# Optimization experiments

Measured on AMD Instinct MI355X. Metric: run time of the kernel, lower is better.

## Reference

```python
import jax, jax.numpy as jnp
import numpy as np
from jax import lax

RATIOS = (0.5, 1.0, 2.0)
SCALES = (8, 16, 32)
BASE = 16
STRIDE = 16
NMS_THRESH = 0.7
N_PRE = 6000   # n_test_pre_nms
N_POST = 300   # n_test_post_nms
MIN_SIZE = 16.0  # min_size * scale (scale=1.0)
NEG = -1e9


def _anchor_base():
    py = px = BASE / 2.0
    ab = np.zeros((len(RATIOS) * len(SCALES), 4), np.float32)
    for i, r in enumerate(RATIOS):
        for j, s in enumerate(SCALES):
            h = BASE * s * np.sqrt(r)
            w = BASE * s * np.sqrt(1.0 / r)
            k = i * len(SCALES) + j
            ab[k] = [py - h / 2.0, px - w / 2.0, py + h / 2.0, px + w / 2.0]
    return ab


def _anchors(hh, ww):
    # enumerate shifted anchors, shape [hh*ww*9, 4] in (y1,x1,y2,x2)
    ab = _anchor_base()
    sy = np.arange(hh, dtype=np.float32) * STRIDE
    sx = np.arange(ww, dtype=np.float32) * STRIDE
    sx, sy = np.meshgrid(sx, sy)
    shift = np.stack([sy.ravel(), sx.ravel(), sy.ravel(), sx.ravel()], axis=1)
    a = (ab[None, :, :] + shift[:, None, :]).reshape(-1, 4).astype(np.float32)
    return jnp.asarray(a)


def _conv(x, w, b, pad):
    y = lax.conv_general_dilated(x, w, (1, 1), [(pad, pad), (pad, pad)],
                                 dimension_numbers=('NCHW', 'OIHW', 'NCHW'))
    return y + b[None, :, None, None]


def _nms(boxes, valid):
    # greedy NMS over score-sorted boxes [N,4]; returns N_POST selected indices (-1 = pad)
    N = boxes.shape[0]
    y1, x1, y2, x2 = boxes[:, 0], boxes[:, 1], boxes[:, 2], boxes[:, 3]
    area = (y2 - y1) * (x2 - x1)
    idx = jnp.arange(N)

    def body(i, sup):
        cur = valid[i] & (~sup[i])
        ih = jnp.clip(jnp.minimum(y2[i], y2) - jnp.maximum(y1[i], y1), 0.0)
        iw = jnp.clip(jnp.minimum(x2[i], x2) - jnp.maximum(x1[i], x1), 0.0)
        inter = ih * iw
        iou = inter / (area[i] + area - inter + 1e-9)
        return sup | (cur & (iou > NMS_THRESH) & (idx > i))

    sup = lax.fori_loop(0, N, body, jnp.zeros((N,), bool))
    kept = valid & (~sup)
    rank = jnp.cumsum(kept) - 1
    sel = jnp.full((N_POST,), -1, jnp.int32)
    sel = sel.at[jnp.where(kept & (rank < N_POST), rank, N_POST)].set(
        jnp.arange(N, dtype=jnp.int32), mode='drop')
    return sel


def setup_inputs() -> dict:
    key = jax.random.key(0)
    ks = jax.random.split(key, 5)
    n, c, hh, ww = 8, 512, 64, 64
    x = jax.random.normal(ks[0], (n, c, hh, ww), jnp.float32)
    # normal_init(mean=0, std=0.01), biases zero
    w1 = 0.01 * jax.random.normal(ks[1], (512, 512, 3, 3), jnp.float32)
    b1 = jnp.zeros((512,), jnp.float32)
    w_score = 0.01 * jax.random.normal(ks[2], (18, 512, 1, 1), jnp.float32)
    b_score = jnp.zeros((18,), jnp.float32)
    w_loc = 0.01 * jax.random.normal(ks[3], (36, 512, 1, 1), jnp.float32)
    b_loc = jnp.zeros((36,), jnp.float32)
    return {"x": x, "w1": w1, "b1": b1, "w_score": w_score, "b_score": b_score,
            "w_loc": w_loc, "b_loc": b_loc, "img_h": 1024, "img_w": 1024}


def reference(x, w1, b1, w_score, b_score, w_loc, b_loc, img_h, img_w):
    n, _, hh, ww = x.shape
    anchor = _anchors(hh, ww)  # [K,4]
    mid = jax.nn.relu(_conv(x, w1, b1, 1))
    rpn_locs = _conv(mid, w_loc, b_loc, 0).transpose(0, 2, 3, 1).reshape(n, -1, 4)  # [n,K,4]
    raw = _conv(mid, w_score, b_score, 0).transpose(0, 2, 3, 1)  # [n,hh,ww,18]
    sm = jax.nn.softmax(raw.reshape(n, hh, ww, -1, 2), axis=-1)
    fg = sm[..., 1].reshape(n, -1)          # [n,K] foreground scores
    rpn_scores = raw.reshape(n, -1, 2)      # pre-softmax, as in original
    # loc2bbox decode
    ah = anchor[:, 2] - anchor[:, 0]
    aw = anchor[:, 3] - anchor[:, 1]
    acy = anchor[:, 0] + 0.5 * ah
    acx = anchor[:, 1] + 0.5 * aw
    dy, dx, dh, dw = (rpn_locs[..., 0], rpn_locs[..., 1], rpn_locs[..., 2], rpn_locs[..., 3])
    cy = dy * ah + acy
    cx = dx * aw + acx
    h = ah * jnp.exp(dh)
    w = aw * jnp.exp(dw)
    fh = jnp.float32(img_h)
    fw = jnp.float32(img_w)
    roi = jnp.stack([jnp.clip(cy - 0.5 * h, 0.0, fh), jnp.clip(cx - 0.5 * w, 0.0, fw),
                     jnp.clip(cy + 0.5 * h, 0.0, fh), jnp.clip(cx + 0.5 * w, 0.0, fw)], axis=-1)
    hs = roi[..., 2] - roi[..., 0]
    ws = roi[..., 3] - roi[..., 1]
    ok = (hs >= MIN_SIZE) & (ws >= MIN_SIZE)
    masked = jnp.where(ok, fg, NEG)
    vals, top = lax.top_k(masked, N_PRE)  # score-descending pre-NMS selection
    boxes = jnp.take_along_axis(roi, top[..., None], axis=1)  # [n,N_PRE,4]
    valid = vals > NEG / 2
    sel = jax.vmap(_nms)(boxes, valid)  # [n,N_POST]
    mask = sel >= 0
    rois = jnp.take_along_axis(boxes, jnp.clip(sel, 0)[..., None], axis=1)
    rois = jnp.where(mask[..., None], rois, 0.0)  # [n,N_POST,4], zero-padded
    roi_indices = jnp.where(mask, jnp.arange(n, dtype=jnp.int32)[:, None], -1)  # -1 = pad
    return (rpn_locs, rpn_scores, rois, roi_indices, anchor)
```

## Files before the change

### kernel.cpp

```cpp
#include <hip/hip_runtime.h>
#include <cstdint>
#include <cstddef>

#define CIN 512
#define NA 36864
#define NPRE 6000
#define NPOST 300
#define CBUF_CAP 8192
#define NWORD 94
#define NEGV -1000000000.0f
#define ISTRIDE 76

#define O_LOCS   0
#define O_SCORES 1179648
#define O_ROIS   1769472
#define O_RIDX   1779072
#define O_ANCH   1781472

__device__ __forceinline__ float fmulr(float a, float b) { return __fmul_rn(a, b); }
__device__ __forceinline__ float faddr(float a, float b) { return __fadd_rn(a, b); }
__device__ __forceinline__ float fsubr(float a, float b) { return __fsub_rn(a, b); }

__device__ __forceinline__ void anchor_for(int a, int pos, float* anc) {
    const double rat[3] = {0.5, 1.0, 2.0};
    const double scl[3] = {8.0, 16.0, 32.0};
    int ri = a / 3, si = a - ri * 3;
    double h = 16.0 * scl[si] * sqrt(rat[ri]);
    double w = 16.0 * scl[si] * sqrt(1.0 / rat[ri]);
    float a0 = (float)(8.0 - h * 0.5);
    float a1 = (float)(8.0 - w * 0.5);
    float a2 = (float)(8.0 + h * 0.5);
    float a3 = (float)(8.0 + w * 0.5);
    int y = pos >> 6, x = pos & 63;
    float sy = (float)(y * 16), sx = (float)(x * 16);
    anc[0] = faddr(a0, sy); anc[1] = faddr(a1, sx);
    anc[2] = faddr(a2, sy); anc[3] = faddr(a3, sx);
}

__device__ __forceinline__ bool decode_box(float4 L, const float* anc, float* box) {
    float ah  = fsubr(anc[2], anc[0]);
    float aw  = fsubr(anc[3], anc[1]);
    float acy = faddr(anc[0], fmulr(0.5f, ah));
    float acx = faddr(anc[1], fmulr(0.5f, aw));
    float cy  = faddr(fmulr(L.x, ah), acy);
    float cx  = faddr(fmulr(L.y, aw), acx);
    float h   = fmulr(ah, expf(L.z));
    float w   = fmulr(aw, expf(L.w));
    float y1 = fminf(fmaxf(fsubr(cy, fmulr(0.5f, h)), 0.0f), 1024.0f);
    float x1 = fminf(fmaxf(fsubr(cx, fmulr(0.5f, w)), 0.0f), 1024.0f);
    float y2 = fminf(fmaxf(faddr(cy, fmulr(0.5f, h)), 0.0f), 1024.0f);
    float x2 = fminf(fmaxf(faddr(cx, fmulr(0.5f, w)), 0.0f), 1024.0f);
    box[0] = y1; box[1] = x1; box[2] = y2; box[3] = x2;
    float hs = fsubr(y2, y1), ws2 = fsubr(x2, x1);
    return (hs >= 16.0f) && (ws2 >= 16.0f);
}

__device__ __forceinline__ unsigned long long mono64(double f) {
    unsigned long long u = (unsigned long long)__double_as_longlong(f);
    return (u & 0x8000000000000000ull) ? ~u : (u | 0x8000000000000000ull);
}

__global__ __launch_bounds__(256) void k_wreord(const float* __restrict__ w1,
                                                float* __restrict__ wr2) {
    __shared__ float tile[64][37];
    const int ct0 = blockIdx.x * 36;
    const int ocb = blockIdx.y;
    const int t = threadIdx.x;
    for (int i = t; i < 64 * 36; i += 256) {
        int orow = i / 36, c = i - orow * 36;
        tile[orow][c] = w1[(size_t)(ocb * 64 + orow) * 4608 + ct0 + c];
    }
    __syncthreads();
    for (int i = t; i < 36 * 64; i += 256) {
        int ct = i >> 6, o = i & 63;
        wr2[((size_t)ocb * 4608 + ct0 + ct) * 64 + o] = tile[o][ct];
    }
}

__global__ __launch_bounds__(256, 2) void k_conv3(const float* __restrict__ x,
                                                  const float* __restrict__ wr2,
                                                  const float* __restrict__ b1,
                                                  float* __restrict__ mid) {
    __shared__ float in_s[8 * 6 * ISTRIDE];
    __shared__ float w_s[8 * 9 * 64];
    const int yb  = blockIdx.x;
    const int ocb = blockIdx.y;
    const int n   = blockIdx.z;
    const int t   = threadIdx.x;
    const int y0  = yb * 4;
    const int tocg = t >> 5;
    const int tx   = t & 31;
    const int r    = tx >> 3;
    const int xo   = (tx & 7) << 3;

    for (int i = t; i < 48 * 8; i += 256) {
        int row = i >> 3, c = i & 7;
        int xi = (c < 4) ? c : 64 + c;
        in_s[row * ISTRIDE + xi] = 0.f;
    }

    int   ilds[3];
    int   ival[3];
    const float* igp[3];
#pragma unroll
    for (int k = 0; k < 3; ++k) {
        int s = t + k * 256;
        int row = s >> 4, col = s & 15;
        int cc = row / 6, rr = row - cc * 6;
        int gy = y0 - 1 + rr;
        ival[k] = (gy >= 0 && gy < 64) ? 1 : 0;
        int gyc = min(max(gy, 0), 63);
        ilds[k] = row * ISTRIDE + 4 + col * 4;
        igp[k]  = x + (((size_t)(n * CIN + cc) * 64 + gyc) * 64 + col * 4);
    }
    const float* wgp = wr2 + (size_t)ocb * (4608 * 64);

    float acc[8][8];
#pragma unroll
    for (int i = 0; i < 8; i++)
#pragma unroll
        for (int j = 0; j < 8; j++) acc[i][j] = 0.f;

    for (int ch = 0; ch < 64; ++ch) {
        const float* wp0 = wgp + (size_t)ch * 4608;
#pragma unroll
        for (int k = 0; k < 4; ++k)
            *(float4*)&w_s[4 * t + 1024 * k] = *(const float4*)(wp0 + 4 * t + 1024 * k);
        if (t < 128)
            *(float4*)&w_s[4 * t + 4096] = *(const float4*)(wp0 + 4 * t + 4096);
#pragma unroll
        for (int k = 0; k < 3; ++k) {
            float4 v = make_float4(0.f, 0.f, 0.f, 0.f);
            if (ival[k]) v = *(const float4*)(igp[k] + (size_t)ch * 32768);
            *(float4*)&in_s[ilds[k]] = v;
        }
        __syncthreads();

        float sub[8][8];
#pragma unroll
        for (int i = 0; i < 8; i++)
#pragma unroll
            for (int j = 0; j < 8; j++) sub[i][j] = 0.f;
#pragma unroll 1
        for (int cc = 0; cc < 8; ++cc) {
#pragma unroll
            for (int dy = 0; dy < 3; ++dy) {
                const float4* ip =
                    (const float4*)&in_s[cc * (6 * ISTRIDE) + (r + dy) * ISTRIDE + xo];
                float4 Q0 = ip[0], Q1 = ip[1], Q2 = ip[2], Q3 = ip[3];
                float in16[16] = {Q0.x, Q0.y, Q0.z, Q0.w, Q1.x, Q1.y, Q1.z, Q1.w,
                                  Q2.x, Q2.y, Q2.z, Q2.w, Q3.x, Q3.y, Q3.z, Q3.w};
#pragma unroll
                for (int dx = 0; dx < 3; ++dx) {
                    const float4* wp =
                        (const float4*)&w_s[cc * 576 + (dy * 3 + dx) * 64 + tocg * 8];
                    float4 W0 = wp[0], W1 = wp[1];
                    float w8[8] = {W0.x, W0.y, W0.z, W0.w, W1.x, W1.y, W1.z, W1.w};
#pragma unroll
                    for (int i = 0; i < 8; i++)
#pragma unroll
                        for (int j = 0; j < 8; j++)
                            sub[i][j] += w8[i] * in16[j + dx + 3];
                }
            }
        }
#pragma unroll
        for (int i = 0; i < 8; i++)
#pragma unroll
            for (int j = 0; j < 8; j++) acc[i][j] += sub[i][j];
        __syncthreads();
    }
    const int ocbase = (ocb << 6) + tocg * 8;
#pragma unroll
    for (int i = 0; i < 8; i++) {
        float bb = b1[ocbase + i];
#pragma unroll
        for (int j = 0; j < 8; j++) {
            float v = fmaxf(acc[i][j] + bb, 0.f);
            mid[((n * CIN + ocbase + i) * 64 + (y0 + r)) * 64 + xo + j] = v;
        }
    }
}

__global__ __launch_bounds__(256) void k_conv1(const float* __restrict__ mid,
                                               const float* __restrict__ wl,
                                               const float* __restrict__ bl,
                                               const float* __restrict__ wsc,
                                               const float* __restrict__ bs,
                                               float* __restrict__ out,
                                               double* __restrict__ fgbuf) {
    __shared__ float in_s[128 * 64];
    __shared__ float w_s[54 * 128];
    const int y = blockIdx.x;
    const int n = blockIdx.y;
    const int t = threadIdx.x;
    const int xx = t & 63, og = t >> 6;
    double accd[14];
#pragma unroll
    for (int k = 0; k < 14; k++) accd[k] = 0.0;

    for (int c0 = 0; c0 < 512; c0 += 128) {
        for (int idx = t; idx < 128 * 64; idx += 256) {
            int cc = idx >> 6, x2 = idx & 63;
            in_s[idx] = mid[((n * CIN + c0 + cc) * 64 + y) * 64 + x2];
        }
        for (int idx = t; idx < 54 * 128; idx += 256) {
            int oc = idx >> 7, cc = idx & 127;
            w_s[idx] = (oc < 36) ? wl[oc * 512 + c0 + cc] : wsc[(oc - 36) * 512 + c0 + cc];
        }
        __syncthreads();
#pragma unroll 1
        for (int cc = 0; cc < 128; ++cc) {
            double iv = (double)in_s[cc * 64 + xx];
#pragma unroll
            for (int k = 0; k < 14; k++) {
                int oc = og * 14 + k;
                if (oc < 54) accd[k] += (double)w_s[oc * 128 + cc] * iv;
            }
        }
        __syncthreads();
    }
    const int pos = y * 64 + xx;
    double sv[14];
#pragma unroll
    for (int k = 0; k < 14; k++) {
        int oc = og * 14 + k;
        if (oc >= 54) break;
        if (oc < 36) {
            double v = accd[k] + (double)bl[oc];
            int a = oc >> 2, cd = oc & 3;
            out[O_LOCS + ((size_t)(n * NA + pos * 9 + a)) * 4 + cd] = (float)v;
        } else {
            sv[k] = accd[k] + (double)bs[oc - 36];
            int c2 = oc - 36, a = c2 >> 1, cls = c2 & 1;
            out[O_SCORES + ((size_t)(n * NA + pos * 9 + a)) * 2 + cls] = (float)sv[k];
        }
    }
#pragma unroll
    for (int k = 0; k < 13; k++) {
        int oc = og * 14 + k;
        if (oc >= 36 && oc < 54 && ((oc - 36) & 1) == 0) {
            double s0 = sv[k], s1 = sv[k + 1];
            double m = fmax(s0, s1);
            double e0 = exp(s0 - m), e1 = exp(s1 - m);
            double fg = e1 / (e0 + e1);
            int a = (oc - 36) >> 1;
            fgbuf[(size_t)n * NA + pos * 9 + a] = fg;
        }
    }
}

__global__ __launch_bounds__(256) void k_keys(const float* __restrict__ out,
                                              const double* __restrict__ fgbuf,
                                              unsigned long long* __restrict__ keys) {
    const int n = blockIdx.x / 144;
    const int i = (blockIdx.x % 144) * 256 + threadIdx.x;
    int pos = i / 9, a = i - pos * 9;
    float anc[4]; anchor_for(a, pos, anc);
    float4 L = *(const float4*)&out[O_LOCS + (size_t)(n * NA + i) * 4];
    float box[4];
    bool ok = decode_box(L, anc, box);
    double f = ok ? fgbuf[(size_t)n * NA + i] : (double)NEGV;
    unsigned long long m = mono64(f);
    keys[(size_t)n * NA + i] =
        (m & 0xFFFFFFFFFFFF0000ull) | (unsigned long long)(0xFFFFu - (unsigned)i);
}

__global__ __launch_bounds__(1024) void k_select(const unsigned long long* __restrict__ keys,
                                                 unsigned long long* __restrict__ kth) {
    __shared__ unsigned int hist[8192];
    __shared__ unsigned int gs[256];
    __shared__ unsigned long long s_pref;
    __shared__ int s_plen, s_rem;
    const int n = blockIdx.x, t = threadIdx.x;
    if (t == 0) { s_pref = 0ull; s_plen = 0; s_rem = NPRE; }
    __syncthreads();
    const int shifts[5] = {51, 38, 25, 12, 0};
    const int widths[5] = {13, 13, 13, 13, 12};
    for (int lev = 0; lev < 5; ++lev) {
        const int nb = 1 << widths[lev];
        for (int b = t; b < nb; b += 1024) hist[b] = 0;
        __syncthreads();
        const unsigned long long pref = s_pref;
        const int plen = s_plen;
        for (int i = t; i < NA; i += 1024) {
            unsigned long long key = keys[(size_t)n * NA + i];
            if (plen == 0 || (key >> (64 - plen)) == pref) {
                unsigned int bin = (unsigned int)((key >> shifts[lev]) & (unsigned)(nb - 1));
                atomicAdd(&hist[bin], 1u);
            }
        }
        __syncthreads();
        const int gsz = nb >> 8;
        if (t < 256) {
            unsigned int s = 0;
            for (int m = 0; m < gsz; m++) s += hist[t * gsz + m];
            gs[t] = s;
        }
        __syncthreads();
        if (t == 0) {
            const unsigned int rem = (unsigned int)s_rem;
            unsigned int acc = 0; int selbin = 0;
            for (int g = 255; g >= 0; --g) {
                if (acc + gs[g] >= rem) {
                    for (int b = g * gsz + gsz - 1; b >= g * gsz; --b) {
                        if (acc + hist[b] >= rem) { selbin = b; break; }
                        acc += hist[b];
                    }
                    break;
                }
                acc += gs[g];
            }
            s_rem = (int)(rem - acc);
            s_pref = (s_pref << widths[lev]) | (unsigned long long)(unsigned)selbin;
            s_plen += widths[lev];
        }
        __syncthreads();
    }
    if (t == 0) kth[n] = s_pref;
}

__global__ void k_compact(const unsigned long long* __restrict__ keys,
                          const unsigned long long* __restrict__ kth,
                          unsigned long long* __restrict__ cbuf,
                          unsigned int* __restrict__ cnt) {
    const int n = blockIdx.x / 144;
    const int i = (blockIdx.x % 144) * 256 + threadIdx.x;
    unsigned long long key = keys[(size_t)n * NA + i];
    if (key >= kth[n]) {
        unsigned int p = atomicAdd(&cnt[n], 1u);
        if (p < CBUF_CAP) cbuf[(size_t)n * CBUF_CAP + p] = key;
    }
}

__global__ __launch_bounds__(1024) void k_sort(const unsigned long long* __restrict__ cbuf,
                                               const float* __restrict__ out,
                                               float* __restrict__ bsort,
                                               unsigned char* __restrict__ vflag) {
    __shared__ unsigned long long arr[CBUF_CAP];
    const int n = blockIdx.x, t = threadIdx.x;
    for (int idx = t; idx < CBUF_CAP; idx += 1024)
        arr[idx] = (idx < NPRE) ? cbuf[(size_t)n * CBUF_CAP + idx] : 0ull;
    __syncthreads();
    for (int k = 2; k <= CBUF_CAP; k <<= 1)
        for (int j = k >> 1; j > 0; j >>= 1) {
            for (int i = t; i < CBUF_CAP; i += 1024) {
                int ixj = i ^ j;
                if (ixj > i) {
                    unsigned long long a = arr[i], b = arr[ixj];
                    bool up = (i & k) == 0;
                    if (up ? (a < b) : (a > b)) { arr[i] = b; arr[ixj] = a; }
                }
            }
            __syncthreads();
        }
    for (int r = t; r < NPRE; r += 1024) {
        unsigned long long key = arr[r];
        unsigned int i = 0xFFFFu - (unsigned int)(key & 0xFFFFull);
        int pos = i / 9, a = i - pos * 9;
        float anc[4]; anchor_for(a, pos, anc);
        float4 L = *(const float4*)&out[O_LOCS + (size_t)(n * NA + i) * 4];
        float box[4];
        bool ok = decode_box(L, anc, box);
        ((float4*)bsort)[(size_t)n * NPRE + r] = make_float4(box[0], box[1], box[2], box[3]);
        vflag[(size_t)n * NPRE + r] = ok ? 1 : 0;
    }
}

__global__ __launch_bounds__(256) void k_mask(const float* __restrict__ bsort,
                                              unsigned long long* __restrict__ masks) {
    __shared__ float4 bx[1024];
    const int n  = blockIdx.z;
    const int jc = blockIdx.y;
    const int i  = blockIdx.x * 256 + threadIdx.x;
    const bool have = i < NPRE;
    float4 bi = make_float4(0, 0, 0, 0); float areai = 0.f;
    if (have) {
        bi = ((const float4*)bsort)[(size_t)n * NPRE + i];
        areai = fmulr(fsubr(bi.z, bi.x), fsubr(bi.w, bi.y));
    }
    const int jn = min(1024, NPRE - jc * 1024);
    for (int jj = threadIdx.x; jj < jn; jj += 256)
        bx[jj] = ((const float4*)bsort)[(size_t)n * NPRE + jc * 1024 + jj];
    __syncthreads();
    for (int w = 0; w < 16; ++w) {
        int gw = jc * 16 + w;
        if (gw >= NWORD) break;
        unsigned long long m = 0ull;
        int jbase = jc * 1024 + w * 64;
        if (have && jbase + 63 > i) {
#pragma unroll 1
            for (int b = 0; b < 64; b++) {
                int j = jbase + b;
                if (j > i && j < NPRE) {
                    float4 bj = bx[w * 64 + b];
                    float ih = fmaxf(fsubr(fminf(bi.z, bj.z), fmaxf(bi.x, bj.x)), 0.f);
                    float iw = fmaxf(fsubr(fminf(bi.w, bj.w), fmaxf(bi.y, bj.y)), 0.f);
                    float inter = fmulr(ih, iw);
                    float areaj = fmulr(fsubr(bj.z, bj.x), fsubr(bj.w, bj.y));
                    float den = faddr(fsubr(faddr(areai, areaj), inter), 1e-9f);
                    float iou = __fdiv_rn(inter, den);
                    if (iou > 0.7f) m |= (1ull << b);
                }
            }
        }
        if (have) masks[((size_t)n * NPRE + i) * NWORD + gw] = m;
    }
}

__global__ __launch_bounds__(128) void k_scan(const unsigned long long* __restrict__ masks,
                                              const unsigned char* __restrict__ vflag,
                                              const float* __restrict__ bsort,
                                              float* __restrict__ out) {
    __shared__ unsigned long long sup[NWORD];
    __shared__ unsigned long long valw[NWORD];
    __shared__ int kept;
    const int n = blockIdx.x, t = threadIdx.x;
    if (t == 0) kept = 0;
    if (t < NWORD) {
        sup[t] = 0ull;
        unsigned long long v = 0ull;
        for (int b = 0; b < 64; b++) {
            int r = t * 64 + b;
            if (r < NPRE && vflag[(size_t)n * NPRE + r]) v |= (1ull << b);
        }
        valw[t] = v;
    }
    __syncthreads();
    for (int i = 0; i < NPRE; ++i) {
        bool keep = ((valw[i >> 6] >> (i & 63)) & 1ull) && !((sup[i >> 6] >> (i & 63)) & 1ull);
        if (keep) {
            if (t < NWORD) sup[t] |= masks[((size_t)n * NPRE + i) * NWORD + t];
            if (t == 0) {
                int r = kept;
                if (r < NPOST) {
                    float4 b4 = ((const float4*)bsort)[(size_t)n * NPRE + i];
                    out[O_ROIS + (size_t)(n * NPOST + r) * 4 + 0] = b4.x;
                    out[O_ROIS + (size_t)(n * NPOST + r) * 4 + 1] = b4.y;
                    out[O_ROIS + (size_t)(n * NPOST + r) * 4 + 2] = b4.z;
                    out[O_ROIS + (size_t)(n * NPOST + r) * 4 + 3] = b4.w;
                    out[O_RIDX + n * NPOST + r] = (float)n;
                }
                kept = r + 1;
            }
            __syncthreads();
            if (kept >= NPOST) break;
        }
    }
    __syncthreads();
    for (int r = kept + t; r < NPOST; r += 128) {
        out[O_ROIS + (size_t)(n * NPOST + r) * 4 + 0] = 0.f;
        out[O_ROIS + (size_t)(n * NPOST + r) * 4 + 1] = 0.f;
        out[O_ROIS + (size_t)(n * NPOST + r) * 4 + 2] = 0.f;
        out[O_ROIS + (size_t)(n * NPOST + r) * 4 + 3] = 0.f;
        out[O_RIDX + n * NPOST + r] = -1.0f;
    }
}

__global__ void k_anchor(float* __restrict__ out) {
    int i = blockIdx.x * 256 + threadIdx.x;
    if (i >= NA) return;
    int pos = i / 9, a = i - pos * 9;
    float anc[4]; anchor_for(a, pos, anc);
    out[O_ANCH + (size_t)i * 4 + 0] = anc[0];
    out[O_ANCH + (size_t)i * 4 + 1] = anc[1];
    out[O_ANCH + (size_t)i * 4 + 2] = anc[2];
    out[O_ANCH + (size_t)i * 4 + 3] = anc[3];
}

extern "C" void kernel_launch(void* const* d_in, const int* in_sizes, int n_in,
                              void* d_out, int out_size, void* d_ws, size_t ws_size,
                              hipStream_t stream) {
    const float* x   = (const float*)d_in[0];
    const float* w1  = (const float*)d_in[1];
    const float* b1  = (const float*)d_in[2];
    const float* wsc = (const float*)d_in[3];
    const float* bsc = (const float*)d_in[4];
    const float* wlc = (const float*)d_in[5];
    const float* blc = (const float*)d_in[6];
    float* out = (float*)d_out;
    char* ws = (char*)d_ws;

    float* wr2                = (float*)(ws + 0);
    float* mid                = (float*)(ws + 9437184);
    double* fgbuf             = (double*)(ws + 76546048);
    unsigned long long* keys  = (unsigned long long*)(ws + 78905344);
    unsigned long long* kth   = (unsigned long long*)(ws + 81264640);
    unsigned int* cnt         = (unsigned int*)(ws + 81265152);
    unsigned long long* cbuf  = (unsigned long long*)(ws + 81265664);
    float* bsort              = (float*)(ws + 81789952);
    unsigned char* vflag      = (unsigned char*)(ws + 82557952);
    unsigned long long* masks = (unsigned long long*)(ws + 82606080);

    hipMemsetAsync(cnt, 0, 8 * 4, stream);

    dim3 gw(128, 8);
    k_wreord<<<gw, 256, 0, stream>>>(w1, wr2);
    dim3 g3(16, 8, 8);
    k_conv3<<<g3, 256, 0, stream>>>(x, wr2, b1, mid);
    dim3 g1(64, 8);
    k_conv1<<<g1, 256, 0, stream>>>(mid, wlc, blc, wsc, bsc, out, fgbuf);
    k_keys<<<1152, 256, 0, stream>>>(out, fgbuf, keys);
    k_select<<<8, 1024, 0, stream>>>(keys, kth);
    k_compact<<<1152, 256, 0, stream>>>(keys, kth, cbuf, cnt);
    k_sort<<<8, 1024, 0, stream>>>(cbuf, out, bsort, vflag);
    dim3 gm(24, 6, 8);
    k_mask<<<gm, 256, 0, stream>>>(bsort, masks);
    k_scan<<<8, 128, 0, stream>>>(masks, vflag, bsort, out);
    k_anchor<<<144, 256, 0, stream>>>(out);
}
```

Measured before the change: 2.998 ms.

## Fuse top-k select/compact/sort kernels and rewrite NMS scan as single-wavefront ballot loop

Merges the radix select, compaction and bitonic sort into one k_topk kernel that reuses a shared-memory union, and folds anchor output into k_keys, which removes several launches and the memset. The radix bin search now uses a parallel suffix scan over group sums in place of a serial loop. The NMS scan kernel becomes one 64-lane wavefront that keeps valid and suppressed bitmasks in registers and uses ballot/ffs to jump straight to the next kept box, avoiding a walk over all 6000 candidates with block syncs. The remaining cost is the 8-block serial tail, and the compaction now uses a global atomic counter that is reset inside the kernel.

After: 3.002 ms. About the same (+0.1%).

```diff
diff --git a/kernel.cpp b/kernel.cpp
--- a/kernel.cpp
+++ b/kernel.cpp
@@ -6,7 +6,7 @@
 #define NA 36864
 #define NPRE 6000
 #define NPOST 300
-#define CBUF_CAP 8192
+#define NARR 8192
 #define NWORD 94
 #define NEGV -1000000000.0f
 #define ISTRIDE 76
@@ -250,39 +250,53 @@
     }
 }
 
-__global__ __launch_bounds__(256) void k_keys(const float* __restrict__ out,
+__global__ __launch_bounds__(256) void k_keys(const float* __restrict__ out_ro,
                                               const double* __restrict__ fgbuf,
-                                              unsigned long long* __restrict__ keys) {
+                                              unsigned long long* __restrict__ keys,
+                                              float* __restrict__ out) {
     const int n = blockIdx.x / 144;
     const int i = (blockIdx.x % 144) * 256 + threadIdx.x;
     int pos = i / 9, a = i - pos * 9;
     float anc[4]; anchor_for(a, pos, anc);
-    float4 L = *(const float4*)&out[O_LOCS + (size_t)(n * NA + i) * 4];
+    float4 L = *(const float4*)&out_ro[O_LOCS + (size_t)(n * NA + i) * 4];
     float box[4];
     bool ok = decode_box(L, anc, box);
     double f = ok ? fgbuf[(size_t)n * NA + i] : (double)NEGV;
     unsigned long long m = mono64(f);
     keys[(size_t)n * NA + i] =
         (m & 0xFFFFFFFFFFFF0000ull) | (unsigned long long)(0xFFFFu - (unsigned)i);
-}
-
-__global__ __launch_bounds__(1024) void k_select(const unsigned long long* __restrict__ keys,
-                                                 unsigned long long* __restrict__ kth) {
-    __shared__ unsigned int hist[8192];
-    __shared__ unsigned int gs[256];
-    __shared__ unsigned long long s_pref;
-    __shared__ int s_plen, s_rem;
+    if (blockIdx.x < 144) {
+        out[O_ANCH + (size_t)i * 4 + 0] = anc[0];
+        out[O_ANCH + (size_t)i * 4 + 1] = anc[1];
+        out[O_ANCH + (size_t)i * 4 + 2] = anc[2];
+        out[O_ANCH + (size_t)i * 4 + 3] = anc[3];
+    }
+}
+
+__global__ __launch_bounds__(1024) void k_topk(const unsigned long long* __restrict__ keys,
+                                               const float* __restrict__ out,
+                                               unsigned int* __restrict__ cntg,
+                                               float* __restrict__ bsort,
+                                               unsigned char* __restrict__ vflag) {
+    __shared__ union SM {
+        unsigned int hist[16384];
+        unsigned long long arr[NARR];
+    } sm;
     const int n = blockIdx.x, t = threadIdx.x;
-    if (t == 0) { s_pref = 0ull; s_plen = 0; s_rem = NPRE; }
+    unsigned int* hist = sm.hist;
+    unsigned int* gs = sm.hist + 8192;
+    unsigned long long* prefp = (unsigned long long*)&sm.hist[8452];
+    if (t == 0) { hist[8448] = NPRE; *prefp = 0ull; }
     __syncthreads();
     const int shifts[5] = {51, 38, 25, 12, 0};
     const int widths[5] = {13, 13, 13, 13, 12};
+    int plen = 0;
     for (int lev = 0; lev < 5; ++lev) {
         const int nb = 1 << widths[lev];
+        const int gsz = nb >> 8;
         for (int b = t; b < nb; b += 1024) hist[b] = 0;
         __syncthreads();
-        const unsigned long long pref = s_pref;
-        const int plen = s_plen;
+        const unsigned long long pref = *prefp;
         for (int i = t; i < NA; i += 1024) {
             unsigned long long key = keys[(size_t)n * NA + i];
             if (plen == 0 || (key >> (64 - plen)) == pref) {
@@ -291,60 +305,57 @@
             }
         }
         __syncthreads();
-        const int gsz = nb >> 8;
         if (t < 256) {
             unsigned int s = 0;
             for (int m = 0; m < gsz; m++) s += hist[t * gsz + m];
             gs[t] = s;
         }
         __syncthreads();
+        for (int off = 1; off < 256; off <<= 1) {
+            unsigned int v = 0;
+            if (t < 256 && t + off < 256) v = gs[t + off];
+            __syncthreads();
+            if (t < 256) gs[t] += v;
+            __syncthreads();
+        }
+        const unsigned int rem = hist[8448];
+        if (t < 256) {
+            unsigned int here = gs[t];
+            unsigned int above = (t == 255) ? 0u : gs[t + 1];
+            if (here >= rem && above < rem) hist[8449] = (unsigned int)t;
+        }
+        __syncthreads();
         if (t == 0) {
-            const unsigned int rem = (unsigned int)s_rem;
-            unsigned int acc = 0; int selbin = 0;
-            for (int g = 255; g >= 0; --g) {
-                if (acc + gs[g] >= rem) {
-                    for (int b = g * gsz + gsz - 1; b >= g * gsz; --b) {
-                        if (acc + hist[b] >= rem) { selbin = b; break; }
-                        acc += hist[b];
-                    }
-                    break;
-                }
-                acc += gs[g];
+            int G = (int)hist[8449];
+            unsigned int acc = (G == 255) ? 0u : gs[G + 1];
+            int selbin = G * gsz;
+            for (int b = G * gsz + gsz - 1; b >= G * gsz; --b) {
+                if (acc + hist[b] >= rem) { selbin = b; break; }
+                acc += hist[b];
             }
-            s_rem = (int)(rem - acc);
-            s_pref = (s_pref << widths[lev]) | (unsigned long long)(unsigned)selbin;
-            s_plen += widths[lev];
-        }
-        __syncthreads();
-    }
-    if (t == 0) kth[n] = s_pref;
-}
-
-__global__ void k_compact(const unsigned long long* __restrict__ keys,
-                          const unsigned long long* __restrict__ kth,
-                          unsigned long long* __restrict__ cbuf,
-                          unsigned int* __restrict__ cnt) {
-    const int n = blockIdx.x / 144;
-    const int i = (blockIdx.x % 144) * 256 + threadIdx.x;
-    unsigned long long key = keys[(size_t)n * NA + i];
-    if (key >= kth[n]) {
-        unsigned int p = atomicAdd(&cnt[n], 1u);
-        if (p < CBUF_CAP) cbuf[(size_t)n * CBUF_CAP + p] = key;
-    }
-}
-
-__global__ __launch_bounds__(1024) void k_sort(const unsigned long long* __restrict__ cbuf,
-                                               const float* __restrict__ out,
-                                               float* __restrict__ bsort,
-                                               unsigned char* __restrict__ vflag) {
-    __shared__ unsigned long long arr[CBUF_CAP];
-    const int n = blockIdx.x, t = threadIdx.x;
-    for (int idx = t; idx < CBUF_CAP; idx += 1024)
-        arr[idx] = (idx < NPRE) ? cbuf[(size_t)n * CBUF_CAP + idx] : 0ull;
+            hist[8448] = rem - acc;
+            *prefp = ((*prefp) << widths[lev]) | (unsigned long long)(unsigned)selbin;
+        }
+        plen += widths[lev];
+        __syncthreads();
+    }
+    const unsigned long long kth = *prefp;
+    if (t == 0) cntg[n] = 0u;
     __syncthreads();
-    for (int k = 2; k <= CBUF_CAP; k <<= 1)
+    unsigned long long* arr = sm.arr;
+    for (int i = t; i < NA; i += 1024) {
+        unsigned long long key = keys[(size_t)n * NA + i];
+        if (key >= kth) {
+            unsigned int p = atomicAdd(&cntg[n], 1u);
+            if (p < NARR) arr[p] = key;
+        }
+    }
+    __syncthreads();
+    for (int idx = NPRE + t; idx < NARR; idx += 1024) arr[idx] = 0ull;
+    __syncthreads();
+    for (int k = 2; k <= NARR; k <<= 1)
         for (int j = k >> 1; j > 0; j >>= 1) {
-            for (int i = t; i < CBUF_CAP; i += 1024) {
+            for (int i = t; i < NARR; i += 1024) {
                 int ixj = i ^ j;
                 if (ixj > i) {
                     unsigned long long a = arr[i], b = arr[ixj];
@@ -408,64 +419,60 @@
     }
 }
 
-__global__ __launch_bounds__(128) void k_scan(const unsigned long long* __restrict__ masks,
-                                              const unsigned char* __restrict__ vflag,
-                                              const float* __restrict__ bsort,
-                                              float* __restrict__ out) {
-    __shared__ unsigned long long sup[NWORD];
-    __shared__ unsigned long long valw[NWORD];
-    __shared__ int kept;
-    const int n = blockIdx.x, t = threadIdx.x;
-    if (t == 0) kept = 0;
-    if (t < NWORD) {
-        sup[t] = 0ull;
-        unsigned long long v = 0ull;
-        for (int b = 0; b < 64; b++) {
-            int r = t * 64 + b;
-            if (r < NPRE && vflag[(size_t)n * NPRE + r]) v |= (1ull << b);
-        }
-        valw[t] = v;
-    }
-    __syncthreads();
-    for (int i = 0; i < NPRE; ++i) {
-        bool keep = ((valw[i >> 6] >> (i & 63)) & 1ull) && !((sup[i >> 6] >> (i & 63)) & 1ull);
-        if (keep) {
-            if (t < NWORD) sup[t] |= masks[((size_t)n * NPRE + i) * NWORD + t];
-            if (t == 0) {
-                int r = kept;
-                if (r < NPOST) {
-                    float4 b4 = ((const float4*)bsort)[(size_t)n * NPRE + i];
-                    out[O_ROIS + (size_t)(n * NPOST + r) * 4 + 0] = b4.x;
-                    out[O_ROIS + (size_t)(n * NPOST + r) * 4 + 1] = b4.y;
-                    out[O_ROIS + (size_t)(n * NPOST + r) * 4 + 2] = b4.z;
-                    out[O_ROIS + (size_t)(n * NPOST + r) * 4 + 3] = b4.w;
-                    out[O_RIDX + n * NPOST + r] = (float)n;
-                }
-                kept = r + 1;
-            }
-            __syncthreads();
-            if (kept >= NPOST) break;
-        }
-    }
-    __syncthreads();
-    for (int r = kept + t; r < NPOST; r += 128) {
+__global__ __launch_bounds__(64) void k_scan(const unsigned long long* __restrict__ masks,
+                                             const unsigned char* __restrict__ vflag,
+                                             const float* __restrict__ bsort,
+                                             float* __restrict__ out) {
+    const int n = blockIdx.x;
+    const int l = threadIdx.x;
+    unsigned long long valw0 = 0ull, valw1 = 0ull;
+    for (int w = 0; w < NWORD; ++w) {
+        int idx = w * 64 + l;
+        bool v = (idx < NPRE) && (vflag[(size_t)n * NPRE + idx] != 0);
+        unsigned long long word = __ballot(v);
+        if (w == l) valw0 = word;
+        if (w == 64 + l) valw1 = word;
+    }
+    unsigned long long sup0 = 0ull, sup1 = 0ull;
+    int kept = 0;
+    while (kept < NPOST) {
+        unsigned long long cand0 = valw0 & ~sup0;
+        unsigned long long cand1 = (l < NWORD - 64) ? (valw1 & ~sup1) : 0ull;
+        unsigned long long b0 = __ballot(cand0 != 0ull);
+        int w; unsigned long long bits;
+        if (b0) {
+            int fl = __ffsll((long long)b0) - 1;
+            w = fl; bits = __shfl(cand0, fl);
+        } else {
+            unsigned long long b1 = __ballot(cand1 != 0ull);
+            if (!b1) break;
+            int fl = __ffsll((long long)b1) - 1;
+            w = 64 + fl; bits = __shfl(cand1, fl);
+        }
+        int i = w * 64 + (__ffsll((long long)bits) - 1);
+        if (l == 0) {
+            float4 b4 = ((const float4*)bsort)[(size_t)n * NPRE + i];
+            out[O_ROIS + (size_t)(n * NPOST + kept) * 4 + 0] = b4.x;
+            out[O_ROIS + (size_t)(n * NPOST + kept) * 4 + 1] = b4.y;
+            out[O_ROIS + (size_t)(n * NPOST + kept) * 4 + 2] = b4.z;
+            out[O_ROIS + (size_t)(n * NPOST + kept) * 4 + 3] = b4.w;
+            out[O_RIDX + n * NPOST + kept] = (float)n;
+        }
+        kept++;
+        if (kept >= NPOST) break;
+        const unsigned long long* mrow = masks + ((size_t)n * NPRE + i) * NWORD;
+        sup0 |= mrow[l];
+        if (l < NWORD - 64) sup1 |= mrow[64 + l];
+        if (w < 64) { if (l == w) sup0 |= (1ull << (i & 63)); }
+        else        { if (l == w - 64) sup1 |= (1ull << (i & 63)); }
+    }
+    for (int r = kept + l; r < NPOST; r += 64) {
         out[O_ROIS + (size_t)(n * NPOST + r) * 4 + 0] = 0.f;
         out[O_ROIS + (size_t)(n * NPOST + r) * 4 + 1] = 0.f;
         out[O_ROIS + (size_t)(n * NPOST + r) * 4 + 2] = 0.f;
         out[O_ROIS + (size_t)(n * NPOST + r) * 4 + 3] = 0.f;
         out[O_RIDX + n * NPOST + r] = -1.0f;
     }
-}
-
-__global__ void k_anchor(float* __restrict__ out) {
-    int i = blockIdx.x * 256 + threadIdx.x;
-    if (i >= NA) return;
-    int pos = i / 9, a = i - pos * 9;
-    float anc[4]; anchor_for(a, pos, anc);
-    out[O_ANCH + (size_t)i * 4 + 0] = anc[0];
-    out[O_ANCH + (size_t)i * 4 + 1] = anc[1];
-    out[O_ANCH + (size_t)i * 4 + 2] = anc[2];
-    out[O_ANCH + (size_t)i * 4 + 3] = anc[3];
 }
 
 extern "C" void kernel_launch(void* const* d_in, const int* in_sizes, int n_in,
@@ -485,14 +492,10 @@
     float* mid                = (float*)(ws + 9437184);
     double* fgbuf             = (double*)(ws + 76546048);
     unsigned long long* keys  = (unsigned long long*)(ws + 78905344);
-    unsigned long long* kth   = (unsigned long long*)(ws + 81264640);
-    unsigned int* cnt         = (unsigned int*)(ws + 81265152);
-    unsigned long long* cbuf  = (unsigned long long*)(ws + 81265664);
+    unsigned int* cntg        = (unsigned int*)(ws + 81265152);
     float* bsort              = (float*)(ws + 81789952);
     unsigned char* vflag      = (unsigned char*)(ws + 82557952);
     unsigned long long* masks = (unsigned long long*)(ws + 82606080);
-
-    hipMemsetAsync(cnt, 0, 8 * 4, stream);
 
     dim3 gw(128, 8);
     k_wreord<<<gw, 256, 0, stream>>>(w1, wr2);
@@ -500,12 +503,9 @@
     k_conv3<<<g3, 256, 0, stream>>>(x, wr2, b1, mid);
     dim3 g1(64, 8);
     k_conv1<<<g1, 256, 0, stream>>>(mid, wlc, blc, wsc, bsc, out, fgbuf);
-    k_keys<<<1152, 256, 0, stream>>>(out, fgbuf, keys);
-    k_select<<<8, 1024, 0, stream>>>(keys, kth);
-    k_compact<<<1152, 256, 0, stream>>>(keys, kth, cbuf, cnt);
-    k_sort<<<8, 1024, 0, stream>>>(cbuf, out, bsort, vflag);
+    k_keys<<<1152, 256, 0, stream>>>(out, fgbuf, keys, out);
+    k_topk<<<8, 1024, 0, stream>>>(keys, out, cntg, bsort, vflag);
     dim3 gm(24, 6, 8);
     k_mask<<<gm, 256, 0, stream>>>(bsort, masks);
-    k_scan<<<8, 128, 0, stream>>>(masks, vflag, bsort, out);
-    k_anchor<<<144, 256, 0, stream>>>(out);
-}
+    k_scan<<<8, 64, 0, stream>>>(masks, vflag, bsort, out);
+}
```
